# Kernel optimization log

Measured on AMD Instinct MI355X. Metric: run time of the kernel, lower is better.

Reference implementation:

```python
import jax, jax.numpy as jnp
import numpy as np
from jax import lax

B, N, C = 8, 16384, 96
ROPE_BASE = 10000.0


def _rope(x):
    """Faithful port of the module's RoPE. x: (b, h, w, c).
    Note: the original computes angles over the h axis but, due to torch
    broadcasting of (h, k_max) against (b, h, w, k_max), the rotation is
    applied along the w axis (valid since h == w)."""
    b, h, w, c = x.shape
    k_max = c // 2
    theta = 1.0 / (ROPE_BASE ** (jnp.arange(k_max, dtype=x.dtype) / k_max))  # (k_max,)
    angles = jnp.arange(h, dtype=x.dtype)[:, None] * theta                  # (h, k_max)
    cos = jnp.cos(angles)[None, None, :, :]  # broadcast over w axis
    sin = jnp.sin(angles)[None, None, :, :]
    xr = x.reshape(b, h, w, k_max, 2)
    xre, xim = xr[..., 0], xr[..., 1]
    ore = xre * cos - xim * sin
    oim = xre * sin + xim * cos
    return jnp.stack([ore, oim], axis=-1).reshape(b, h, w, c)


def setup_inputs() -> dict:
    key = jax.random.key(0)
    ks = jax.random.split(key, 5)
    return {
        "x": jax.random.normal(ks[0], (B, N, C), dtype=jnp.float32),
        "qk_w": jax.random.normal(ks[1], (2 * C, C), dtype=jnp.float32) * 0.05,
        "qk_b": jax.random.normal(ks[2], (2 * C,), dtype=jnp.float32) * 0.02,
        "lepe_w": jax.random.normal(ks[3], (C, 1, 3, 3), dtype=jnp.float32) * 0.1,
        "lepe_b": jax.random.normal(ks[4], (C,), dtype=jnp.float32) * 0.02,
        "num_heads": 4,
    }


def reference(x, qk_w, qk_b, lepe_w, lepe_b, num_heads):
    b, n, c = x.shape
    h = w = int(round(n ** 0.5))
    d = c // num_heads
    inv_sqrt_n = float(n) ** (-0.5)

    qk = x @ qk_w.T + qk_b                        # (b, n, 2c)
    q = jax.nn.elu(qk[..., :c]) + 1.0             # (b, n, c)
    k = jax.nn.elu(qk[..., c:]) + 1.0
    v = x

    q_rope = _rope(q.reshape(b, h, w, c)).reshape(b, n, num_heads, d).transpose(0, 2, 1, 3)
    k_rope = _rope(k.reshape(b, h, w, c)).reshape(b, n, num_heads, d).transpose(0, 2, 1, 3)
    qh = q.reshape(b, n, num_heads, d).transpose(0, 2, 1, 3)  # (b, H, n, d)
    kh = k.reshape(b, n, num_heads, d).transpose(0, 2, 1, 3)
    vh = v.reshape(b, n, num_heads, d).transpose(0, 2, 1, 3)

    k_mean = kh.mean(axis=2, keepdims=True)                         # (b, H, 1, d)
    z = 1.0 / (jnp.einsum('bhnd,bhmd->bhnm', qh, k_mean) + 1e-6)    # (b, H, n, 1)
    kv = jnp.einsum('bhnd,bhne->bhde', k_rope * inv_sqrt_n, vh * inv_sqrt_n)  # (b, H, d, d)
    out = jnp.einsum('bhnd,bhde->bhne', q_rope, kv) * z             # (b, H, n, d)
    out = out.transpose(0, 2, 1, 3).reshape(b, n, c)

    # LePE: depthwise 3x3 conv on v laid out as (b, c, h, w)
    v_img = vh.transpose(0, 2, 1, 3).reshape(b, h, w, c).transpose(0, 3, 1, 2)
    lepe = lax.conv_general_dilated(
        v_img, lepe_w, window_strides=(1, 1), padding='SAME',
        feature_group_count=c, dimension_numbers=('NCHW', 'OIHW', 'NCHW'))
    lepe = lepe + lepe_b[None, :, None, None]
    return out + lepe.transpose(0, 2, 3, 1).reshape(b, n, c)
```

## Files before the change

kernel.cpp:

```cpp
#include <hip/hip_runtime.h>


#define NLINE 16384
#define CCH 96
#define KTP 136
#define QSP 104
#define OUTP 98
#define THETA_COEF 0.2768273412406135f
#define LOG2_2PI   2.6514961294723187f

typedef __attribute__((ext_vector_type(4))) float f32x4;
typedef __attribute__((ext_vector_type(8))) short bf16x8;
typedef __attribute__((ext_vector_type(2))) __fp16 fp16x2;

__device__ __forceinline__ unsigned short f2bf(float f) {
  unsigned int u = __float_as_uint(f);
  u += 0x7FFFu + ((u >> 16) & 1u);
  return (unsigned short)(u >> 16);
}
__device__ __forceinline__ float bf2f(unsigned short h) {
  return __uint_as_float(((unsigned int)h) << 16);
}
__device__ __forceinline__ bf16x8 pack_bf8(f32x4 v0, f32x4 v1) {
  bf16x8 r;
  r[0] = (short)f2bf(v0.x); r[1] = (short)f2bf(v0.y);
  r[2] = (short)f2bf(v0.z); r[3] = (short)f2bf(v0.w);
  r[4] = (short)f2bf(v1.x); r[5] = (short)f2bf(v1.y);
  r[6] = (short)f2bf(v1.z); r[7] = (short)f2bf(v1.w);
  return r;
}

__global__ void prep_w2(const float* __restrict__ qkw,
                        unsigned short* __restrict__ wfrag,
                        float* __restrict__ kvT) {
  int idx = blockIdx.x * 256 + threadIdx.x;
  if (idx < 25344) kvT[idx] = 0.0f;
  if (idx < 2304) {
    int u = idx;
    int lane = u & 63;
    int nt = (u >> 6) % 6;
    int rest = u / 384;
    int kk = rest % 3, half = rest / 3;
    int lr = lane & 15, q4 = lane >> 4;
    const float* src = qkw + (half * 96 + nt * 16 + lr) * 96 + kk * 32 + q4 * 8;
    unsigned short* dst = wfrag + (size_t)u * 8;
#pragma unroll
    for (int j = 0; j < 8; ++j) dst[j] = f2bf(src[j]);
  }
}

__global__ __launch_bounds__(256, 4) void la_k1(
    const float* __restrict__ x, const unsigned short* __restrict__ wfrag,
    const float* __restrict__ qkb, float* __restrict__ kvT,
    float* __restrict__ ksum_g, float* __restrict__ kvp,
    float* __restrict__ ksump)
{
  const int tid  = threadIdx.x;
  const int b    = blockIdx.x >> 7;
  const int tile = blockIdx.x & 127;

  __shared__ alignas(16) unsigned short kqt[96 * KTP];
  __shared__ float ksum_s[96];

  if (tid < 96) ksum_s[tid] = 0.0f;
  __syncthreads();

  const int wave = tid >> 6;
  const int lane = tid & 63;
  const int lr   = lane & 15;
  const int q4   = lane >> 4;
  const int row0 = wave * 32;
  const float* xb = x + ((size_t)b * NLINE + (size_t)tile * 128) * CCH;

  bf16x8 afr[2][3];
#pragma unroll
  for (int mt = 0; mt < 2; ++mt)
#pragma unroll
    for (int kk = 0; kk < 3; ++kk) {
      const float* ap = xb + (row0 + mt * 16 + lr) * CCH + kk * 32 + q4 * 8;
      afr[mt][kk] = pack_bf8(((const f32x4*)ap)[0], ((const f32x4*)ap)[1]);
    }

  float biasv[6];
#pragma unroll
  for (int nt = 0; nt < 6; ++nt) biasv[nt] = qkb[96 + nt * 16 + lr];

  f32x4 acc[2][6];
#pragma unroll
  for (int mt = 0; mt < 2; ++mt)
#pragma unroll
    for (int nt = 0; nt < 6; ++nt) acc[mt][nt] = (f32x4){0.f, 0.f, 0.f, 0.f};

#pragma unroll
  for (int kk = 0; kk < 3; ++kk) {
#pragma unroll
    for (int nt = 0; nt < 6; ++nt) {
      bf16x8 bf = *(const bf16x8*)&wfrag[(size_t)(((3 + kk) * 6 + nt) * 64 + lane) * 8];
      acc[0][nt] = __builtin_amdgcn_mfma_f32_16x16x32_bf16(afr[0][kk], bf, acc[0][nt], 0, 0, 0);
      acc[1][nt] = __builtin_amdgcn_mfma_f32_16x16x32_bf16(afr[1][kk], bf, acc[1][nt], 0, 0, 0);
    }
  }

  const int odd = lr & 1;
#pragma unroll
  for (int nt = 0; nt < 6; ++nt) {
    const int col = nt * 16 + lr;
    const float threv = exp2f(-THETA_COEF * (float)(col >> 1) - LOG2_2PI);
    float csum = 0.0f;
    float vv[2][4];
#pragma unroll
    for (int mt = 0; mt < 2; ++mt)
#pragma unroll
      for (int rg = 0; rg < 4; ++rg) {
        float v = acc[mt][nt][rg] + biasv[nt];
        v = (v > 0.0f) ? (v + 1.0f) : __expf(v);
        csum += v;
        vv[mt][rg] = v;
      }
    atomicAdd(&ksum_s[col], csum);
#pragma unroll
    for (int mt = 0; mt < 2; ++mt) {
      unsigned long long pk = 0;
#pragma unroll
      for (int rg = 0; rg < 4; ++rg) {
        float p = __shfl_xor(vv[mt][rg], 1);
        int r = row0 + mt * 16 + q4 * 4 + rg;
        float rev = (float)r * threv;
        float sn = __builtin_amdgcn_sinf(rev);
        float cn = __builtin_amdgcn_cosf(rev);
        float o = odd ? (p * sn + vv[mt][rg] * cn)
                      : (vv[mt][rg] * cn - p * sn);
        pk |= (unsigned long long)f2bf(o) << (16 * rg);
      }
      *(unsigned long long*)&kqt[col * KTP + row0 + mt * 16 + q4 * 4] = pk;
    }
  }
  __syncthreads();

  if (tid < 96) {
    if (kvp) ksump[((size_t)b * 128 + tile) * 96 + tid] = ksum_s[tid];
    else     atomicAdd(&ksum_g[b * 96 + tid], ksum_s[tid]);
  }

  const int h = wave;
  f32x4 kvacc[2][2];
#pragma unroll
  for (int mt = 0; mt < 2; ++mt)
#pragma unroll
    for (int nt = 0; nt < 2; ++nt) kvacc[mt][nt] = (f32x4){0.f, 0.f, 0.f, 0.f};

#pragma unroll
  for (int kk = 0; kk < 4; ++kk) {
    const int rbase = kk * 32 + q4 * 8;
    bf16x8 ka[2], vb[2];
#pragma unroll
    for (int mt = 0; mt < 2; ++mt) {
      int c = 24 * h + mt * 16 + lr; if (c > 95) c = 95;
      ka[mt] = *(const bf16x8*)&kqt[c * KTP + rbase];
    }
#pragma unroll
    for (int nt = 0; nt < 2; ++nt) {
      int c = 24 * h + nt * 16 + lr; if (c > 95) c = 95;
#pragma unroll
      for (int j = 0; j < 8; ++j)
        vb[nt][j] = (short)f2bf(xb[(rbase + j) * CCH + c]);
    }
#pragma unroll
    for (int mt = 0; mt < 2; ++mt)
#pragma unroll
      for (int nt = 0; nt < 2; ++nt)
        kvacc[mt][nt] = __builtin_amdgcn_mfma_f32_16x16x32_bf16(ka[mt], vb[nt], kvacc[mt][nt], 0, 0, 0);
  }

  if (kvp) {
    float* dst = kvp + ((size_t)(b * 128 + tile) * 4 + h) * 576;
#pragma unroll
    for (int mt = 0; mt < 2; ++mt)
#pragma unroll
      for (int rg = 0; rg < 4; ++rg) {
        int d = mt * 16 + q4 * 4 + rg;
        if (d < 24) {
#pragma unroll
          for (int nt = 0; nt < 2; ++nt) {
            int e = nt * 16 + lr;
            if (e < 24) dst[d * 24 + e] = kvacc[mt][nt][rg];
          }
        }
      }
  } else {
    const float inv_n = 1.0f / 16384.0f;
    float* kvbT = kvT + ((size_t)b * 4 + h) * 768;
#pragma unroll
    for (int mt = 0; mt < 2; ++mt)
#pragma unroll
      for (int rg = 0; rg < 4; ++rg) {
        int d = mt * 16 + q4 * 4 + rg;
        if (d < 24) {
#pragma unroll
          for (int nt = 0; nt < 2; ++nt) {
            int e = nt * 16 + lr;
            if (e < 24) atomicAdd(&kvbT[e * 32 + d], kvacc[mt][nt][rg] * inv_n);
          }
        }
      }
  }
}

__global__ void la_reduce(const float* __restrict__ kvp,
                          const float* __restrict__ ksump,
                          float* __restrict__ kvT,
                          float* __restrict__ ksum_g) {
  int i = blockIdx.x * 256 + threadIdx.x;
  if (i < 18432) {
    int bh = i / 576, de = i - bh * 576;
    int b = bh >> 2, h = bh & 3;
    int d = de / 24, e = de - d * 24;
    const float* src = kvp + ((size_t)b * 512 + h) * 576 + de;
    float s0 = 0.f, s1 = 0.f, s2 = 0.f, s3 = 0.f;
#pragma unroll 4
    for (int p = 0; p < 128; p += 4) {
      s0 += src[(p + 0) * 2304];
      s1 += src[(p + 1) * 2304];
      s2 += src[(p + 2) * 2304];
      s3 += src[(p + 3) * 2304];
    }
    kvT[(size_t)bh * 768 + e * 32 + d] = ((s0 + s1) + (s2 + s3)) * (1.0f / 16384.0f);
  } else if (i < 19200) {
    int j = i - 18432;
    int b = j / 96, c = j - b * 96;
    const float* src = ksump + (size_t)b * 128 * 96 + c;
    float s0 = 0.f, s1 = 0.f, s2 = 0.f, s3 = 0.f;
#pragma unroll 4
    for (int p = 0; p < 128; p += 4) {
      s0 += src[(p + 0) * 96];
      s1 += src[(p + 1) * 96];
      s2 += src[(p + 2) * 96];
      s3 += src[(p + 3) * 96];
    }
    ksum_g[b * 96 + c] = (s0 + s1) + (s2 + s3);
  }
}

__global__ __launch_bounds__(256, 8) void la_k2(
    const float* __restrict__ x, const unsigned short* __restrict__ wfrag,
    const float* __restrict__ qkb, const float* __restrict__ lepe_w,
    const float* __restrict__ lepe_b, const float* __restrict__ kvT,
    const float* __restrict__ ksum_g, float* __restrict__ out)
{
  const int tid = threadIdx.x;
  const int b   = blockIdx.x & 7;
  const int seg = blockIdx.x >> 3;
  const int y   = seg >> 1;

  __shared__ alignas(16) unsigned short qs[64 * QSP];
  __shared__ alignas(16) float zs[64 * 4];
  __shared__ alignas(16) float lepe_s[9 * 96];

  for (int i = tid; i < 864; i += 256) {
    int ch = i / 9, tap = i % 9;
    lepe_s[tap * 96 + ch] = lepe_w[i];
  }

  const int wave = tid >> 6;
  const int lane = tid & 63;
  const int lr   = lane & 15;
  const int q4   = lane >> 4;

  float biasv[6], kmv[6];
#pragma unroll
  for (int nt = 0; nt < 6; ++nt) {
    biasv[nt] = qkb[nt * 16 + lr];
    kmv[nt]   = ksum_g[b * 96 + nt * 16 + lr];
  }

  const float* xb = x + ((size_t)b * NLINE + (size_t)seg * 64) * CCH;
  bf16x8 afrag[3];
#pragma unroll
  for (int kk = 0; kk < 3; ++kk) {
    const float* ap = xb + (wave * 16 + lr) * CCH + kk * 32 + q4 * 8;
    afrag[kk] = pack_bf8(((const f32x4*)ap)[0], ((const f32x4*)ap)[1]);
  }

  f32x4 acc[6];
#pragma unroll
  for (int nt = 0; nt < 6; ++nt) acc[nt] = (f32x4){0.f, 0.f, 0.f, 0.f};
#pragma unroll
  for (int kk = 0; kk < 3; ++kk) {
#pragma unroll
    for (int nt = 0; nt < 6; ++nt) {
      bf16x8 bf = *(const bf16x8*)&wfrag[(size_t)((kk * 6 + nt) * 64 + lane) * 8];
      acc[nt] = __builtin_amdgcn_mfma_f32_16x16x32_bf16(afrag[kk], bf, acc[nt], 0, 0, 0);
    }
  }

  const int odd = lr & 1;
  const int t0  = wave * 16 + q4 * 4;
  const int xwb = ((seg & 1) << 6) + t0;
  float d0[4], d1[4], d2[4], d3[4];
#pragma unroll
  for (int rg = 0; rg < 4; ++rg) { d0[rg] = 0.f; d1[rg] = 0.f; d2[rg] = 0.f; d3[rg] = 0.f; }

#pragma unroll
  for (int nt = 0; nt < 6; ++nt) {
    const int col = nt * 16 + lr;
    const float threv = exp2f(-THETA_COEF * (float)(col >> 1) - LOG2_2PI);
    float vv[4];
#pragma unroll
    for (int rg = 0; rg < 4; ++rg) {
      float v = acc[nt][rg] + biasv[nt];
      v = (v > 0.0f) ? (v + 1.0f) : __expf(v);
      vv[rg] = v;
    }
#pragma unroll
    for (int rg = 0; rg < 4; ++rg) {
      float p = vv[rg] * kmv[nt];
      if (nt == 0)      d0[rg] += p;
      else if (nt == 1) { if (lr < 8) d0[rg] += p; else d1[rg] += p; }
      else if (nt == 2) d1[rg] += p;
      else if (nt == 3) d2[rg] += p;
      else if (nt == 4) { if (lr < 8) d2[rg] += p; else d3[rg] += p; }
      else              d3[rg] += p;
    }
#pragma unroll
    for (int rg = 0; rg < 4; ++rg) {
      float p = __shfl_xor(vv[rg], 1);
      float rev = (float)(xwb + rg) * threv;
      float sn = __builtin_amdgcn_sinf(rev);
      float cn = __builtin_amdgcn_cosf(rev);
      float o = odd ? (p * sn + vv[rg] * cn)
                    : (vv[rg] * cn - p * sn);
      qs[(t0 + rg) * QSP + col] = f2bf(o);
    }
  }

  {
    const float inv_n = 1.0f / 16384.0f;
#pragma unroll
    for (int rg = 0; rg < 4; ++rg) {
      float s0 = d0[rg], s1 = d1[rg], s2 = d2[rg], s3 = d3[rg];
#pragma unroll
      for (int m = 1; m <= 8; m <<= 1) {
        s0 += __shfl_xor(s0, m);
        s1 += __shfl_xor(s1, m);
        s2 += __shfl_xor(s2, m);
        s3 += __shfl_xor(s3, m);
      }
      if (lr == 0) {
        f32x4 zv = { 1.0f / (s0 * inv_n + 1e-6f), 1.0f / (s1 * inv_n + 1e-6f),
                     1.0f / (s2 * inv_n + 1e-6f), 1.0f / (s3 * inv_n + 1e-6f) };
        *(f32x4*)&zs[(t0 + rg) * 4] = zv;
      }
    }
  }
  __syncthreads();

  const int h2 = wave;
  bf16x8 qa[4];
#pragma unroll
  for (int m = 0; m < 4; ++m) {
    qa[m] = *(const bf16x8*)&qs[(16 * m + lr) * QSP + 24 * h2 + q4 * 8];
    if (q4 == 3) {
#pragma unroll
      for (int j = 0; j < 8; ++j) qa[m][j] = 0;
    }
  }
  bf16x8 kb[2];
  {
    const float* kvhT = kvT + ((size_t)b * 4 + h2) * 768;
#pragma unroll
    for (int n = 0; n < 2; ++n) {
      int e = n * 16 + lr;
      int er = (e < 24) ? e : 0;
      const f32x4* p = (const f32x4*)&kvhT[er * 32 + q4 * 8];
      kb[n] = pack_bf8(p[0], p[1]);
    }
  }
  f32x4 c2[4][2];
#pragma unroll
  for (int m = 0; m < 4; ++m)
#pragma unroll
    for (int n = 0; n < 2; ++n) c2[m][n] = (f32x4){0.f, 0.f, 0.f, 0.f};
#pragma unroll
  for (int m = 0; m < 4; ++m)
#pragma unroll
    for (int n = 0; n < 2; ++n)
      c2[m][n] = __builtin_amdgcn_mfma_f32_16x16x32_bf16(qa[m], kb[n], c2[m][n], 0, 0, 0);

  __syncthreads();

  __fp16* outs = (__fp16*)qs;
  {
    float lb0 = lepe_b[24 * h2 + lr];
    float lb1 = (lr < 8) ? lepe_b[24 * h2 + 16 + lr] : 0.0f;
#pragma unroll
    for (int m = 0; m < 4; ++m)
#pragma unroll
      for (int rg = 0; rg < 4; ++rg) {
        int t = 16 * m + q4 * 4 + rg;
        float zv = zs[t * 4 + h2];
        outs[t * OUTP + 24 * h2 + lr] = (__fp16)(c2[m][0][rg] * zv + lb0);
        if (lr < 8)
          outs[t * OUTP + 24 * h2 + 16 + lr] = (__fp16)(c2[m][1][rg] * zv + lb1);
      }
  }
  __syncthreads();

  float* ob = out + ((size_t)b * NLINE + (size_t)seg * 64) * CCH;
  const float* xg = x + (size_t)b * NLINE * CCH;
#pragma unroll
  for (int k = 0; k < 6; ++k) {
    int idx = tid + 256 * k;
    int tl = idx / 24, c4 = idx % 24;
    int ch0 = c4 * 4;
    int xw = ((seg & 1) << 6) + tl;

    fp16x2 p0 = *(const fp16x2*)&outs[tl * OUTP + ch0];
    fp16x2 p1 = *(const fp16x2*)&outs[tl * OUTP + ch0 + 2];
    float r0 = (float)p0[0], r1 = (float)p0[1];
    float r2 = (float)p1[0], r3 = (float)p1[1];

#pragma unroll
    for (int dy = 0; dy < 3; ++dy) {
      int yy = y + dy - 1;
      if (yy < 0 || yy > 127) continue;
      const float* rowp = xg + ((size_t)yy * 128) * CCH;
#pragma unroll
      for (int dx = 0; dx < 3; ++dx) {
        int xx = xw + dx - 1;
        if (xx < 0 || xx > 127) continue;
        f32x4 v = *(const f32x4*)(rowp + xx * CCH + ch0);
        f32x4 w = *(const f32x4*)&lepe_s[(dy * 3 + dx) * 96 + ch0];
        r0 += w.x * v.x;
        r1 += w.y * v.y;
        r2 += w.z * v.z;
        r3 += w.w * v.w;
      }
    }
    f32x4 o = { r0, r1, r2, r3 };
    ((f32x4*)ob)[idx] = o;
  }
}

extern "C" void kernel_launch(void* const* d_in, const int* in_sizes, int n_in,
                              void* d_out, int out_size, void* d_ws, size_t ws_size,
                              hipStream_t stream) {
  const float* x      = (const float*)d_in[0];
  const float* qkw    = (const float*)d_in[1];
  const float* qkb    = (const float*)d_in[2];
  const float* lepe_w = (const float*)d_in[3];
  const float* lepe_b = (const float*)d_in[4];
  float* out = (float*)d_out;

  unsigned short* wfrag = (unsigned short*)d_ws;
  float* kvT    = (float*)((char*)d_ws + 36864);
  float* ksum_g = kvT + 24576;
  float* kvp    = ksum_g + 768;
  float* ksump  = kvp + 2359296;

  const bool partial = (ws_size >= 9968640u);

  prep_w2<<<dim3(100), dim3(256), 0, stream>>>(qkw, wfrag, kvT);
  la_k1<<<dim3(1024), dim3(256), 0, stream>>>(x, wfrag, qkb, kvT, ksum_g,
                                              partial ? kvp : nullptr,
                                              partial ? ksump : nullptr);
  if (partial)
    la_reduce<<<dim3(75), dim3(256), 0, stream>>>(kvp, ksump, kvT, ksum_g);
  la_k2<<<dim3(2048), dim3(256), 0, stream>>>(x, wfrag, qkb, lepe_w, lepe_b,
                                              kvT, ksum_g, out);
}
```

Before: 170.9 us.

## Split k1 into 64-row blocks with more partials, and transpose LePE weight layout

Adds a la_k1h kernel that handles 64-row segments with 2048 blocks and higher occupancy (launch bounds 8). Each block writes partial kv and ksum results, and la_reduce now sums 256 partials. This path is used when the workspace is large enough. The LePE weights in shared memory are also re-laid out as channel-strided to change the LDS access pattern. In exchange, twice as many partials are written to and reduced from global memory, and the new path depends on the workspace size.

```diff
diff --git a/kernel.cpp b/kernel.cpp
--- a/kernel.cpp
+++ b/kernel.cpp
@@ -3,7 +3,8 @@
 
 #define NLINE 16384
 #define CCH 96
-#define KTP 136
+#define KTPF 136
+#define KTPH 72
 #define QSP 104
 #define OUTP 98
 #define THETA_COEF 0.2768273412406135f
@@ -49,6 +50,130 @@
   }
 }
 
+__global__ __launch_bounds__(256, 8) void la_k1h(
+    const float* __restrict__ x, const unsigned short* __restrict__ wfrag,
+    const float* __restrict__ qkb, float* __restrict__ kvp,
+    float* __restrict__ ksump)
+{
+  const int tid  = threadIdx.x;
+  const int b    = blockIdx.x >> 8;
+  const int seg  = blockIdx.x & 255;
+  const int half = seg & 1;
+
+  __shared__ alignas(16) unsigned short kqt[96 * KTPH];
+  __shared__ float ksum_s[96];
+
+  if (tid < 96) ksum_s[tid] = 0.0f;
+  __syncthreads();
+
+  const int wv   = tid >> 6;
+  const int lane = tid & 63;
+  const int lr   = lane & 15;
+  const int q4   = lane >> 4;
+  const float* xb = x + ((size_t)b * NLINE + (size_t)seg * 64) * CCH;
+
+  bf16x8 afr[3];
+#pragma unroll
+  for (int kk = 0; kk < 3; ++kk) {
+    const float* ap = xb + (wv * 16 + lr) * CCH + kk * 32 + q4 * 8;
+    afr[kk] = pack_bf8(((const f32x4*)ap)[0], ((const f32x4*)ap)[1]);
+  }
+
+  float biasv[6];
+#pragma unroll
+  for (int nt = 0; nt < 6; ++nt) biasv[nt] = qkb[96 + nt * 16 + lr];
+
+  f32x4 acc[6];
+#pragma unroll
+  for (int nt = 0; nt < 6; ++nt) acc[nt] = (f32x4){0.f, 0.f, 0.f, 0.f};
+#pragma unroll
+  for (int kk = 0; kk < 3; ++kk) {
+#pragma unroll
+    for (int nt = 0; nt < 6; ++nt) {
+      bf16x8 bf = *(const bf16x8*)&wfrag[(size_t)(((3 + kk) * 6 + nt) * 64 + lane) * 8];
+      acc[nt] = __builtin_amdgcn_mfma_f32_16x16x32_bf16(afr[kk], bf, acc[nt], 0, 0, 0);
+    }
+  }
+
+  const int odd = lr & 1;
+#pragma unroll
+  for (int nt = 0; nt < 6; ++nt) {
+    const int col = nt * 16 + lr;
+    const float threv = exp2f(-THETA_COEF * (float)(col >> 1) - LOG2_2PI);
+    float csum = 0.0f;
+    float vv[4];
+#pragma unroll
+    for (int rg = 0; rg < 4; ++rg) {
+      float v = acc[nt][rg] + biasv[nt];
+      v = (v > 0.0f) ? (v + 1.0f) : __expf(v);
+      csum += v;
+      vv[rg] = v;
+    }
+    atomicAdd(&ksum_s[col], csum);
+    unsigned long long pk = 0;
+#pragma unroll
+    for (int rg = 0; rg < 4; ++rg) {
+      float p = __shfl_xor(vv[rg], 1);
+      int r = half * 64 + wv * 16 + q4 * 4 + rg;
+      float rev = (float)r * threv;
+      float sn = __builtin_amdgcn_sinf(rev);
+      float cn = __builtin_amdgcn_cosf(rev);
+      float o = odd ? (p * sn + vv[rg] * cn)
+                    : (vv[rg] * cn - p * sn);
+      pk |= (unsigned long long)f2bf(o) << (16 * rg);
+    }
+    *(unsigned long long*)&kqt[col * KTPH + wv * 16 + q4 * 4] = pk;
+  }
+  __syncthreads();
+
+  if (tid < 96) ksump[((size_t)b * 256 + seg) * 96 + tid] = ksum_s[tid];
+
+  const int h = wv;
+  f32x4 kvacc[2][2];
+#pragma unroll
+  for (int mt = 0; mt < 2; ++mt)
+#pragma unroll
+    for (int nt = 0; nt < 2; ++nt) kvacc[mt][nt] = (f32x4){0.f, 0.f, 0.f, 0.f};
+
+#pragma unroll
+  for (int kk = 0; kk < 2; ++kk) {
+    const int rbase = kk * 32 + q4 * 8;
+    bf16x8 ka[2], vb[2];
+#pragma unroll
+    for (int mt = 0; mt < 2; ++mt) {
+      int c = 24 * h + mt * 16 + lr; if (c > 95) c = 95;
+      ka[mt] = *(const bf16x8*)&kqt[c * KTPH + rbase];
+    }
+#pragma unroll
+    for (int nt = 0; nt < 2; ++nt) {
+      int c = 24 * h + nt * 16 + lr; if (c > 95) c = 95;
+#pragma unroll
+      for (int j = 0; j < 8; ++j)
+        vb[nt][j] = (short)f2bf(xb[(rbase + j) * CCH + c]);
+    }
+#pragma unroll
+    for (int mt = 0; mt < 2; ++mt)
+#pragma unroll
+      for (int nt = 0; nt < 2; ++nt)
+        kvacc[mt][nt] = __builtin_amdgcn_mfma_f32_16x16x32_bf16(ka[mt], vb[nt], kvacc[mt][nt], 0, 0, 0);
+  }
+
+  float* dst = kvp + ((size_t)(b * 256 + seg) * 4 + h) * 576;
+#pragma unroll
+  for (int mt = 0; mt < 2; ++mt)
+#pragma unroll
+    for (int rg = 0; rg < 4; ++rg) {
+      int d = mt * 16 + q4 * 4 + rg;
+      if (d < 24) {
+#pragma unroll
+        for (int nt = 0; nt < 2; ++nt) {
+          int e = nt * 16 + lr;
+          if (e < 24) dst[d * 24 + e] = kvacc[mt][nt][rg];
+        }
+      }
+    }
+}
+
 __global__ __launch_bounds__(256, 4) void la_k1(
     const float* __restrict__ x, const unsigned short* __restrict__ wfrag,
     const float* __restrict__ qkb, float* __restrict__ kvT,
@@ -59,7 +184,7 @@
   const int b    = blockIdx.x >> 7;
   const int tile = blockIdx.x & 127;
 
-  __shared__ alignas(16) unsigned short kqt[96 * KTP];
+  __shared__ alignas(16) unsigned short kqt[96 * KTPF];
   __shared__ float ksum_s[96];
 
   if (tid < 96) ksum_s[tid] = 0.0f;
@@ -132,7 +257,7 @@
                       : (vv[mt][rg] * cn - p * sn);
         pk |= (unsigned long long)f2bf(o) << (16 * rg);
       }
-      *(unsigned long long*)&kqt[col * KTP + row0 + mt * 16 + q4 * 4] = pk;
+      *(unsigned long long*)&kqt[col * KTPF + row0 + mt * 16 + q4 * 4] = pk;
     }
   }
   __syncthreads();
@@ -156,7 +281,7 @@
 #pragma unroll
     for (int mt = 0; mt < 2; ++mt) {
       int c = 24 * h + mt * 16 + lr; if (c > 95) c = 95;
-      ka[mt] = *(const bf16x8*)&kqt[c * KTP + rbase];
+      ka[mt] = *(const bf16x8*)&kqt[c * KTPF + rbase];
     }
 #pragma unroll
     for (int nt = 0; nt < 2; ++nt) {
@@ -209,29 +334,27 @@
 __global__ void la_reduce(const float* __restrict__ kvp,
                           const float* __restrict__ ksump,
                           float* __restrict__ kvT,
-                          float* __restrict__ ksum_g) {
+                          float* __restrict__ ksum_g, int P) {
   int i = blockIdx.x * 256 + threadIdx.x;
   if (i < 18432) {
     int bh = i / 576, de = i - bh * 576;
     int b = bh >> 2, h = bh & 3;
     int d = de / 24, e = de - d * 24;
-    const float* src = kvp + ((size_t)b * 512 + h) * 576 + de;
+    const float* src = kvp + ((size_t)b * P * 4 + h) * 576 + de;
     float s0 = 0.f, s1 = 0.f, s2 = 0.f, s3 = 0.f;
-#pragma unroll 4
-    for (int p = 0; p < 128; p += 4) {
-      s0 += src[(p + 0) * 2304];
-      s1 += src[(p + 1) * 2304];
-      s2 += src[(p + 2) * 2304];
-      s3 += src[(p + 3) * 2304];
+    for (int p = 0; p < P; p += 4) {
+      s0 += src[(size_t)(p + 0) * 2304];
+      s1 += src[(size_t)(p + 1) * 2304];
+      s2 += src[(size_t)(p + 2) * 2304];
+      s3 += src[(size_t)(p + 3) * 2304];
     }
     kvT[(size_t)bh * 768 + e * 32 + d] = ((s0 + s1) + (s2 + s3)) * (1.0f / 16384.0f);
   } else if (i < 19200) {
     int j = i - 18432;
     int b = j / 96, c = j - b * 96;
-    const float* src = ksump + (size_t)b * 128 * 96 + c;
+    const float* src = ksump + (size_t)b * P * 96 + c;
     float s0 = 0.f, s1 = 0.f, s2 = 0.f, s3 = 0.f;
-#pragma unroll 4
-    for (int p = 0; p < 128; p += 4) {
+    for (int p = 0; p < P; p += 4) {
       s0 += src[(p + 0) * 96];
       s1 += src[(p + 1) * 96];
       s2 += src[(p + 2) * 96];
@@ -254,11 +377,11 @@
 
   __shared__ alignas(16) unsigned short qs[64 * QSP];
   __shared__ alignas(16) float zs[64 * 4];
-  __shared__ alignas(16) float lepe_s[9 * 96];
+  __shared__ float lepe_s[9 * 96];
 
   for (int i = tid; i < 864; i += 256) {
     int ch = i / 9, tap = i % 9;
-    lepe_s[tap * 96 + ch] = lepe_w[i];
+    lepe_s[tap * 96 + (ch & 3) * 24 + (ch >> 2)] = lepe_w[i];
   }
 
   const int wave = tid >> 6;
@@ -429,11 +552,11 @@
         int xx = xw + dx - 1;
         if (xx < 0 || xx > 127) continue;
         f32x4 v = *(const f32x4*)(rowp + xx * CCH + ch0);
-        f32x4 w = *(const f32x4*)&lepe_s[(dy * 3 + dx) * 96 + ch0];
-        r0 += w.x * v.x;
-        r1 += w.y * v.y;
-        r2 += w.z * v.z;
-        r3 += w.w * v.w;
+        const float* wp = &lepe_s[(dy * 3 + dx) * 96 + c4];
+        r0 += wp[0]  * v.x;
+        r1 += wp[24] * v.y;
+        r2 += wp[48] * v.z;
+        r3 += wp[72] * v.w;
       }
     }
     f32x4 o = { r0, r1, r2, r3 };
@@ -455,16 +578,22 @@
   float* kvT    = (float*)((char*)d_ws + 36864);
   float* ksum_g = kvT + 24576;
   float* kvp    = ksum_g + 768;
-  float* ksump  = kvp + 2359296;
-
-  const bool partial = (ws_size >= 9968640u);
+  float* ksump  = kvp + 4718592;
+  float* ksumpF = kvp + 2359296;
 
   prep_w2<<<dim3(100), dim3(256), 0, stream>>>(qkw, wfrag, kvT);
-  la_k1<<<dim3(1024), dim3(256), 0, stream>>>(x, wfrag, qkb, kvT, ksum_g,
-                                              partial ? kvp : nullptr,
-                                              partial ? ksump : nullptr);
-  if (partial)
-    la_reduce<<<dim3(75), dim3(256), 0, stream>>>(kvp, ksump, kvT, ksum_g);
+
+  if (ws_size >= 19799040u) {
+    la_k1h<<<dim3(2048), dim3(256), 0, stream>>>(x, wfrag, qkb, kvp, ksump);
+    la_reduce<<<dim3(75), dim3(256), 0, stream>>>(kvp, ksump, kvT, ksum_g, 256);
+  } else if (ws_size >= 9968640u) {
+    la_k1<<<dim3(1024), dim3(256), 0, stream>>>(x, wfrag, qkb, kvT, ksum_g,
+                                                kvp, ksumpF);
+    la_reduce<<<dim3(75), dim3(256), 0, stream>>>(kvp, ksumpF, kvT, ksum_g, 128);
+  } else {
+    la_k1<<<dim3(1024), dim3(256), 0, stream>>>(x, wfrag, qkb, kvT, ksum_g,
+                                                nullptr, nullptr);
+  }
   la_k2<<<dim3(2048), dim3(256), 0, stream>>>(x, wfrag, qkb, lepe_w, lepe_b,
                                               kvT, ksum_g, out);
 }
```

After: 184.0 us. 7.7% more time.
